# Kernel optimization log

Hardware: AMD Instinct MI355X
Metric: run time of the kernel (lower is better)

## Reference

```python
import jax, jax.numpy as jnp
import numpy as np
from jax import lax

B, T, N, F, K = 8, 16, 1024, 128, 4


def setup_inputs() -> dict:
    key = jax.random.key(0)
    k1, k2, k3, k4 = jax.random.split(key, 4)
    x = jax.random.normal(k1, (B, T, N, F), dtype=jnp.float32)
    # shift operator scaled so its spectral radius is ~1 (stable powers L^1..L^K)
    L = jax.random.normal(k2, (N, N), dtype=jnp.float32) / jnp.sqrt(jnp.float32(N))
    # xavier_uniform with relu gain: limit = gain * sqrt(6/(fan_in+fan_out))
    gain = jnp.sqrt(jnp.float32(2.0))
    lim = gain * jnp.sqrt(6.0 / (F + F))
    W = jax.random.uniform(k3, (K, F, F), dtype=jnp.float32, minval=-lim, maxval=lim)
    H = jax.random.uniform(k4, (K, F, F), dtype=jnp.float32, minval=-lim, maxval=lim)
    return {"x": x, "L": L, "W": W, "H": H}


def reference(x, L, W, H):
    """Recurrent graph-polynomial filter.

    h_t = relu( sum_{k=0}^{K-1} L^{k+1} @ (x_t @ W[k] + h_{t-1} @ H[k]) ), h_{-1}=0.
    Matches the torch loop where alpha_k starts at L and is multiplied by L each tap.
    """
    Kt = W.shape[0]
    # powers L^1 .. L^K, stacked [K, N, N]
    pows = [L]
    for _ in range(1, Kt):
        pows.append(pows[-1] @ L)
    Lp = jnp.stack(pows)

    def step(h, x_t):
        # x_t, h: [B, N, F]
        s = jnp.einsum('bnf,kfg->kbng', x_t, W) + jnp.einsum('bnf,kfg->kbng', h, H)
        z = jnp.einsum('knm,kbmg->bng', Lp, s)
        h_new = jax.nn.relu(z)
        return h_new, h_new

    xT = jnp.swapaxes(x, 0, 1)          # [T, B, N, F]
    h0 = jnp.zeros_like(x[:, 0])        # [B, N, F]
    _, outs = lax.scan(step, h0, xT)    # [T, B, N, F]
    return jnp.swapaxes(outs, 0, 1)     # [B, T, N, F]
```

## Files before the change

kernel.cpp:

```cpp
#include <hip/hip_runtime.h>
#include <stdint.h>


typedef __bf16 bf16_t;
typedef __bf16 bf16x4 __attribute__((ext_vector_type(4)));
typedef __bf16 bf16x8 __attribute__((ext_vector_type(8)));
typedef float  f32x4  __attribute__((ext_vector_type(4)));

__device__ __forceinline__ void gload_lds16(const void* g, void* l) {
    __builtin_amdgcn_global_load_lds(
        (const __attribute__((address_space(1))) void*)g,
        (__attribute__((address_space(3))) void*)l,
        16, 0, 0);
}


__global__ void k_convert_x(const float* __restrict__ xin,
                            bf16_t* __restrict__ xb, int n4) {
    int i = blockIdx.x * 256 + threadIdx.x;
    int stride = gridDim.x * 256;
    for (; i < n4; i += stride) {
        float4 v = reinterpret_cast<const float4*>(xin)[i];
        bf16x4 o = { (bf16_t)v.x, (bf16_t)v.y, (bf16_t)v.z, (bf16_t)v.w };
        reinterpret_cast<bf16x4*>(xb)[i] = o;
    }
}

__global__ void k_setup_L(const float* __restrict__ L,
                          bf16_t* __restrict__ Lcat,
                          bf16_t* __restrict__ Lt) {
    int idx = blockIdx.x * 256 + threadIdx.x;
    int n = idx >> 10, m = idx & 1023;
    float v = L[idx];
    Lcat[n * 4096 + m] = (bf16_t)v;
    Lt[m * 1024 + n]   = (bf16_t)v;
}

__global__ void k_setup_WH(const float* __restrict__ W,
                           const float* __restrict__ H,
                           bf16_t* __restrict__ WHT) {
    int idx = blockIdx.x * 256 + threadIdx.x;
    int k = idx >> 14, f = (idx >> 7) & 127, g = idx & 127;
    WHT[(k * 128 + g) * 256 + f]       = (bf16_t)W[idx];
    WHT[(k * 128 + g) * 256 + 128 + f] = (bf16_t)H[idx];
}


__global__ __launch_bounds__(256)
void k_combine(const float* __restrict__ Zp,
               bf16_t* __restrict__ h, float* __restrict__ out, int t) {
    int i = blockIdx.x * 256 + threadIdx.x;
    int n  = i >> 8;
    int cg = (i & 255) * 4;
    size_t o = (size_t)n * 1024 + cg;
    float4 v0 = *reinterpret_cast<const float4*>(Zp + o);
    float4 v1 = *reinterpret_cast<const float4*>(Zp + 1048576 + o);
    float4 v2 = *reinterpret_cast<const float4*>(Zp + 2097152 + o);
    float4 v3 = *reinterpret_cast<const float4*>(Zp + 3145728 + o);
    float4 s;
    s.x = fmaxf(v0.x + v1.x + v2.x + v3.x, 0.f);
    s.y = fmaxf(v0.y + v1.y + v2.y + v3.y, 0.f);
    s.z = fmaxf(v0.z + v1.z + v2.z + v3.z, 0.f);
    s.w = fmaxf(v0.w + v1.w + v2.w + v3.w, 0.f);
    int b = cg >> 7, g = cg & 127;
    size_t ho = (size_t)b * 131072 + (size_t)n * 128 + g;
    bf16x4 hb = { (bf16_t)s.x, (bf16_t)s.y, (bf16_t)s.z, (bf16_t)s.w };
    *reinterpret_cast<bf16x4*>(h + ho) = hb;
    *reinterpret_cast<float4*>(out + (size_t)b * 2097152
                                   + (size_t)t * 131072
                                   + (size_t)n * 128 + g) = s;
}

template<int BM, int BN, int EPI, int BADDR, int ZK>
__global__ __launch_bounds__(256)
void k_gemm(const bf16_t* __restrict__ A, int lda,
            const bf16_t* __restrict__ BT, int ldbt,
            const bf16_t* __restrict__ B2,
            int Ktot,
            bf16_t* __restrict__ Cb, float* __restrict__ Cf,
            int ldc, int t)
{
    constexpr int BK = 64;
    constexpr int WM = BM / 2, WN = BN / 2;
    constexpr int MF = WM / 16, NF = WN / 16;
    constexpr int ACH = BM * 8;
    constexpr int BCH = BN * 8;

    __shared__ __align__(16) bf16_t As[2][BM * BK];
    __shared__ __align__(16) bf16_t Bs[2][BN * BK];

    const int tid  = threadIdx.x;
    const int lane = tid & 63;
    const int wave = tid >> 6;
    const int wm = wave >> 1, wn = wave & 1;
    const int m0 = blockIdx.y * BM;
    const int c0 = blockIdx.x * BN;
    const int kb_ = blockIdx.z;

    const bf16_t* Ap = (EPI == 1) ? (A + kb_ * 128 * 256) : A;

    f32x4 acc[MF][NF] = {};

    const int NT = Ktot / BK;

    auto stage = [&](int bufi, int kt) {
        const int q0 = kt * BK + (ZK > 0 ? kb_ * ZK : 0);
        #pragma unroll
        for (int i = 0; i < ACH / 256; ++i) {
            int chunk = i * 256 + tid;
            int off = chunk * 16;
            int row = off >> 7;
            int kel = ((off ^ ((row & 7) << 4)) & 127) >> 1;
            const bf16_t* src = Ap + (size_t)(m0 + row) * lda + (q0 + kel);
            gload_lds16(src, (char*)(&As[bufi][0]) + off);
        }
        #pragma unroll
        for (int i = 0; i < BCH / 256; ++i) {
            int chunk = i * 256 + tid;
            int off = chunk * 16;
            int row = off >> 7;
            int kel = ((off ^ ((row & 7) << 4)) & 127) >> 1;
            int c = c0 + row;
            const bf16_t* src;
            if (BADDR == 0) {
                src = BT + (size_t)c * ldbt + (q0 + kel);
            } else {
                int f = q0 + kel;
                if (q0 < 128) {
                    src = BT + (size_t)(c >> 10) * 2097152
                             + (size_t)t * 131072
                             + (size_t)(c & 1023) * 128 + f;
                } else {
                    src = B2 + (size_t)c * 128 + (f - 128);
                }
            }
            gload_lds16(src, (char*)(&Bs[bufi][0]) + off);
        }
    };

    stage(0, 0);
    asm volatile("s_waitcnt vmcnt(0)" ::: "memory");
    __syncthreads();

    for (int kt = 0; kt < NT; ++kt) {
        int cur = kt & 1;
        if (kt + 1 < NT) stage(cur ^ 1, kt + 1);

        #pragma unroll
        for (int kk = 0; kk < 2; ++kk) {
            bf16x8 af[MF], bfr[NF];
            const int klane = (kk * 32 + (lane >> 4) * 8) * 2;
            #pragma unroll
            for (int mf = 0; mf < MF; ++mf) {
                int row = wm * WM + mf * 16 + (lane & 15);
                int bo = (row * 128 + klane) ^ ((row & 7) << 4);
                af[mf] = *reinterpret_cast<const bf16x8*>(
                             (const char*)(&As[cur][0]) + bo);
            }
            #pragma unroll
            for (int nf = 0; nf < NF; ++nf) {
                int row = wn * WN + nf * 16 + (lane & 15);
                int bo = (row * 128 + klane) ^ ((row & 7) << 4);
                bfr[nf] = *reinterpret_cast<const bf16x8*>(
                              (const char*)(&Bs[cur][0]) + bo);
            }
            #pragma unroll
            for (int mf = 0; mf < MF; ++mf)
                #pragma unroll
                for (int nf = 0; nf < NF; ++nf)
                    acc[mf][nf] = __builtin_amdgcn_mfma_f32_16x16x32_bf16(
                        af[mf], bfr[nf], acc[mf][nf], 0, 0, 0);
        }

        asm volatile("s_waitcnt vmcnt(0)" ::: "memory");
        __syncthreads();
    }

    #pragma unroll
    for (int mf = 0; mf < MF; ++mf) {
        #pragma unroll
        for (int nf = 0; nf < NF; ++nf) {
            f32x4 v = acc[mf][nf];
            int col   = c0 + wn * WN + nf * 16 + (lane & 15);
            int rbase = m0 + wm * WM + mf * 16 + ((lane >> 4) * 4);
            #pragma unroll
            for (int r = 0; r < 4; ++r) {
                int row = rbase + r;
                float val = v[r];
                if (EPI == 0) {
                    Cb[(size_t)row * ldc + col] = (bf16_t)val;
                } else if (EPI == 1) {
                    Cb[(size_t)(col >> 10) * 524288 + (size_t)row * 4096
                       + (size_t)kb_ * 1024 + (col & 1023)] = (bf16_t)val;
                } else if (EPI == 2) {
                    val = fmaxf(val, 0.f);
                    int b = col >> 7, g = col & 127;
                    Cb[(size_t)b * 131072 + (size_t)row * 128 + g] = (bf16_t)val;
                    Cf[(size_t)b * 2097152 + (size_t)t * 131072
                       + (size_t)row * 128 + g] = val;
                } else {
                    Cf[(size_t)kb_ * 1048576 + (size_t)row * 1024 + col] = val;
                }
            }
        }
    }
}


extern "C" void kernel_launch(void* const* d_in, const int* in_sizes, int n_in,
                              void* d_out, int out_size, void* d_ws, size_t ws_size,
                              hipStream_t stream) {
    const float* x = (const float*)d_in[0];
    const float* L = (const float*)d_in[1];
    const float* W = (const float*)d_in[2];
    const float* H = (const float*)d_in[3];
    float* out = (float*)d_out;

    char* ws = (char*)d_ws;
    bf16_t* xb   = (bf16_t*)(ws);
    bf16_t* Lcat = (bf16_t*)(ws + 33554432);
    bf16_t* Lt   = (bf16_t*)(ws + 41943040);
    bf16_t* WHT  = (bf16_t*)(ws + 44040192);
    bf16_t* Sbuf = (bf16_t*)(ws + 44302336);
    bf16_t* h    = (bf16_t*)(ws + 52690944);
    float*  Zp   = (float*) (ws + 54788096);
    if (ws_size < 54788096u) return;
    const bool bigws = (ws_size >= 71565312u);

    hipMemsetAsync(h, 0, 2097152, stream);
    k_convert_x<<<4096, 256, 0, stream>>>(x, xb, 16777216 / 4);
    k_setup_L <<<4096, 256, 0, stream>>>(L, Lcat, Lt);
    k_setup_WH<<<256, 256, 0, stream>>>(W, H, WHT);

    for (int p = 1; p < 4; ++p) {
        k_gemm<64, 64, 0, 0, 0><<<dim3(16, 16, 1), 256, 0, stream>>>(
            Lcat + (p - 1) * 1024, 4096, Lt, 1024, nullptr,
            1024, Lcat + p * 1024, nullptr, 4096, 0);
    }

    for (int t = 0; t < 16; ++t) {
        k_gemm<64, 128, 1, 1, 0><<<dim3(64, 2, 4), 256, 0, stream>>>(
            WHT, 256, xb, 0, h,
            256, Sbuf, nullptr, 0, t);
        if (bigws) {
            k_gemm<64, 128, 3, 0, 1024><<<dim3(8, 16, 4), 256, 0, stream>>>(
                Lcat, 4096, Sbuf, 4096, nullptr,
                1024, nullptr, Zp, 0, t);
            k_combine<<<1024, 256, 0, stream>>>(Zp, h, out, t);
        } else {
            k_gemm<64, 128, 2, 0, 0><<<dim3(8, 16, 1), 256, 0, stream>>>(
                Lcat, 4096, Sbuf, 4096, nullptr,
                4096, h, out, 0, t);
        }
    }
}
```

Before: 544.2 us.

## Load GEMM fragments directly from global memory with register double-buffering and XCD swizzle

```diff
diff --git a/kernel.cpp b/kernel.cpp
--- a/kernel.cpp
+++ b/kernel.cpp
@@ -6,13 +6,6 @@
 typedef __bf16 bf16x4 __attribute__((ext_vector_type(4)));
 typedef __bf16 bf16x8 __attribute__((ext_vector_type(8)));
 typedef float  f32x4  __attribute__((ext_vector_type(4)));
-
-__device__ __forceinline__ void gload_lds16(const void* g, void* l) {
-    __builtin_amdgcn_global_load_lds(
-        (const __attribute__((address_space(1))) void*)g,
-        (__attribute__((address_space(3))) void*)l,
-        16, 0, 0);
-}
 
 
 __global__ void k_convert_x(const float* __restrict__ xin,
@@ -71,109 +64,112 @@
                                    + (size_t)n * 128 + g) = s;
 }
 
-template<int BM, int BN, int EPI, int BADDR, int ZK>
+template<int BM, int BN, int GX, int GY, int GZ, int KTOT,
+         int EPI, int BADDR, int ZK, int DEC>
 __global__ __launch_bounds__(256)
 void k_gemm(const bf16_t* __restrict__ A, int lda,
             const bf16_t* __restrict__ BT, int ldbt,
             const bf16_t* __restrict__ B2,
-            int Ktot,
             bf16_t* __restrict__ Cb, float* __restrict__ Cf,
             int ldc, int t)
 {
     constexpr int BK = 64;
     constexpr int WM = BM / 2, WN = BN / 2;
     constexpr int MF = WM / 16, NF = WN / 16;
-    constexpr int ACH = BM * 8;
-    constexpr int BCH = BN * 8;
-
-    __shared__ __align__(16) bf16_t As[2][BM * BK];
-    __shared__ __align__(16) bf16_t Bs[2][BN * BK];
+    constexpr int NT = KTOT / BK;
+    constexpr int NWG = GX * GY * GZ;
 
     const int tid  = threadIdx.x;
     const int lane = tid & 63;
     const int wave = tid >> 6;
     const int wm = wave >> 1, wn = wave & 1;
-    const int m0 = blockIdx.y * BM;
-    const int c0 = blockIdx.x * BN;
-    const int kb_ = blockIdx.z;
+
+    const int id  = blockIdx.x;
+    const int swz = (id & 7) * (NWG / 8) + (id >> 3);
+    int bx, by, bz;
+    if (DEC == 0) {
+        bx = swz % GX; by = (swz / GX) % GY; bz = swz / (GX * GY);
+    } else {
+        by = swz % GY; bz = (swz / GY) % GZ; bx = swz / (GY * GZ);
+    }
+
+    const int m0 = by * BM;
+    const int c0 = bx * BN;
+    const int kb_ = bz;
 
     const bf16_t* Ap = (EPI == 1) ? (A + kb_ * 128 * 256) : A;
+    const int q0base = (ZK > 0) ? kb_ * ZK : 0;
+
+    const int lane15 = lane & 15;
+    const int ksub   = (lane >> 4) * 8;
+
+    uint32_t offA[MF];
+    #pragma unroll
+    for (int mf = 0; mf < MF; ++mf) {
+        uint32_t row = (uint32_t)(m0 + wm * WM + mf * 16 + lane15);
+        offA[mf] = row * (uint32_t)lda + (uint32_t)(q0base + ksub);
+    }
+    uint32_t offB[NF], offBx[NF], offBh[NF];
+    #pragma unroll
+    for (int nf = 0; nf < NF; ++nf) {
+        uint32_t c = (uint32_t)(c0 + wn * WN + nf * 16 + lane15);
+        if (BADDR == 0) {
+            offB[nf] = c * (uint32_t)ldbt + (uint32_t)(q0base + ksub);
+            offBx[nf] = 0; offBh[nf] = 0;
+        } else {
+            offB[nf] = 0;
+            offBx[nf] = (c >> 10) * 2097152u + (uint32_t)t * 131072u
+                      + (c & 1023u) * 128u + (uint32_t)ksub;
+            offBh[nf] = c * 128u + (uint32_t)ksub;
+        }
+    }
+
+    auto ldA = [&](int mf, int tile, int kk) -> bf16x8 {
+        return *reinterpret_cast<const bf16x8*>(
+            Ap + offA[mf] + (uint32_t)(tile * 64 + kk * 32));
+    };
+    auto ldB = [&](int nf, int tile, int kk) -> bf16x8 {
+        if constexpr (BADDR == 0) {
+            return *reinterpret_cast<const bf16x8*>(
+                BT + offB[nf] + (uint32_t)(tile * 64 + kk * 32));
+        } else {
+            if (tile < NT / 2)
+                return *reinterpret_cast<const bf16x8*>(
+                    BT + offBx[nf] + (uint32_t)(tile * 64 + kk * 32));
+            return *reinterpret_cast<const bf16x8*>(
+                B2 + offBh[nf] + (uint32_t)((tile - NT / 2) * 64 + kk * 32));
+        }
+    };
 
     f32x4 acc[MF][NF] = {};
-
-    const int NT = Ktot / BK;
-
-    auto stage = [&](int bufi, int kt) {
-        const int q0 = kt * BK + (ZK > 0 ? kb_ * ZK : 0);
-        #pragma unroll
-        for (int i = 0; i < ACH / 256; ++i) {
-            int chunk = i * 256 + tid;
-            int off = chunk * 16;
-            int row = off >> 7;
-            int kel = ((off ^ ((row & 7) << 4)) & 127) >> 1;
-            const bf16_t* src = Ap + (size_t)(m0 + row) * lda + (q0 + kel);
-            gload_lds16(src, (char*)(&As[bufi][0]) + off);
-        }
-        #pragma unroll
-        for (int i = 0; i < BCH / 256; ++i) {
-            int chunk = i * 256 + tid;
-            int off = chunk * 16;
-            int row = off >> 7;
-            int kel = ((off ^ ((row & 7) << 4)) & 127) >> 1;
-            int c = c0 + row;
-            const bf16_t* src;
-            if (BADDR == 0) {
-                src = BT + (size_t)c * ldbt + (q0 + kel);
-            } else {
-                int f = q0 + kel;
-                if (q0 < 128) {
-                    src = BT + (size_t)(c >> 10) * 2097152
-                             + (size_t)t * 131072
-                             + (size_t)(c & 1023) * 128 + f;
-                } else {
-                    src = B2 + (size_t)c * 128 + (f - 128);
-                }
-            }
-            gload_lds16(src, (char*)(&Bs[bufi][0]) + off);
-        }
-    };
-
-    stage(0, 0);
-    asm volatile("s_waitcnt vmcnt(0)" ::: "memory");
-    __syncthreads();
-
-    for (int kt = 0; kt < NT; ++kt) {
-        int cur = kt & 1;
-        if (kt + 1 < NT) stage(cur ^ 1, kt + 1);
-
+    bf16x8 a0[MF][2], b0[NF][2], a1[MF][2], b1[NF][2];
+
+    auto loadT = [&](bf16x8 (&fa)[MF][2], bf16x8 (&fb)[NF][2], int tile) {
         #pragma unroll
         for (int kk = 0; kk < 2; ++kk) {
-            bf16x8 af[MF], bfr[NF];
-            const int klane = (kk * 32 + (lane >> 4) * 8) * 2;
-            #pragma unroll
-            for (int mf = 0; mf < MF; ++mf) {
-                int row = wm * WM + mf * 16 + (lane & 15);
-                int bo = (row * 128 + klane) ^ ((row & 7) << 4);
-                af[mf] = *reinterpret_cast<const bf16x8*>(
-                             (const char*)(&As[cur][0]) + bo);
-            }
-            #pragma unroll
-            for (int nf = 0; nf < NF; ++nf) {
-                int row = wn * WN + nf * 16 + (lane & 15);
-                int bo = (row * 128 + klane) ^ ((row & 7) << 4);
-                bfr[nf] = *reinterpret_cast<const bf16x8*>(
-                              (const char*)(&Bs[cur][0]) + bo);
-            }
+            #pragma unroll
+            for (int mf = 0; mf < MF; ++mf) fa[mf][kk] = ldA(mf, tile, kk);
+            #pragma unroll
+            for (int nf = 0; nf < NF; ++nf) fb[nf][kk] = ldB(nf, tile, kk);
+        }
+    };
+    auto mfmaT = [&](bf16x8 (&fa)[MF][2], bf16x8 (&fb)[NF][2]) {
+        #pragma unroll
+        for (int kk = 0; kk < 2; ++kk)
             #pragma unroll
             for (int mf = 0; mf < MF; ++mf)
                 #pragma unroll
                 for (int nf = 0; nf < NF; ++nf)
                     acc[mf][nf] = __builtin_amdgcn_mfma_f32_16x16x32_bf16(
-                        af[mf], bfr[nf], acc[mf][nf], 0, 0, 0);
-        }
-
-        asm volatile("s_waitcnt vmcnt(0)" ::: "memory");
-        __syncthreads();
+                        fa[mf][kk], fb[nf][kk], acc[mf][nf], 0, 0, 0);
+    };
+
+    loadT(a0, b0, 0);
+    for (int kt = 0; kt < NT; kt += 2) {
+        loadT(a1, b1, kt + 1);
+        mfmaT(a0, b0);
+        if (kt + 2 < NT) loadT(a0, b0, kt + 2);
+        mfmaT(a1, b1);
     }
 
     #pragma unroll
@@ -181,7 +177,7 @@
         #pragma unroll
         for (int nf = 0; nf < NF; ++nf) {
             f32x4 v = acc[mf][nf];
-            int col   = c0 + wn * WN + nf * 16 + (lane & 15);
+            int col   = c0 + wn * WN + nf * 16 + lane15;
             int rbase = m0 + wm * WM + mf * 16 + ((lane >> 4) * 4);
             #pragma unroll
             for (int r = 0; r < 4; ++r) {
@@ -233,24 +229,24 @@
     k_setup_WH<<<256, 256, 0, stream>>>(W, H, WHT);
 
     for (int p = 1; p < 4; ++p) {
-        k_gemm<64, 64, 0, 0, 0><<<dim3(16, 16, 1), 256, 0, stream>>>(
+        k_gemm<64, 64, 16, 16, 1, 1024, 0, 0, 0, 0><<<256, 256, 0, stream>>>(
             Lcat + (p - 1) * 1024, 4096, Lt, 1024, nullptr,
-            1024, Lcat + p * 1024, nullptr, 4096, 0);
+            Lcat + p * 1024, nullptr, 4096, 0);
     }
 
     for (int t = 0; t < 16; ++t) {
-        k_gemm<64, 128, 1, 1, 0><<<dim3(64, 2, 4), 256, 0, stream>>>(
+        k_gemm<64, 128, 64, 2, 4, 256, 1, 1, 0, 1><<<512, 256, 0, stream>>>(
             WHT, 256, xb, 0, h,
-            256, Sbuf, nullptr, 0, t);
+            Sbuf, nullptr, 0, t);
         if (bigws) {
-            k_gemm<64, 128, 3, 0, 1024><<<dim3(8, 16, 4), 256, 0, stream>>>(
+            k_gemm<64, 128, 8, 16, 4, 1024, 3, 0, 1024, 0><<<512, 256, 0, stream>>>(
                 Lcat, 4096, Sbuf, 4096, nullptr,
-                1024, nullptr, Zp, 0, t);
+                nullptr, Zp, 0, t);
             k_combine<<<1024, 256, 0, stream>>>(Zp, h, out, t);
         } else {
-            k_gemm<64, 128, 2, 0, 0><<<dim3(8, 16, 1), 256, 0, stream>>>(
+            k_gemm<64, 128, 8, 16, 1, 4096, 2, 0, 0, 0><<<128, 256, 0, stream>>>(
                 Lcat, 4096, Sbuf, 4096, nullptr,
-                4096, h, out, 0, t);
-        }
-    }
-}
+                h, out, 0, t);
+        }
+    }
+}
```

Measured after the change: 1.127 ms. 107% more time.

## Switch GEMMs to 32x32 MFMA, larger tiles, 8-way split-K and XCD swizzle

Applied to the files above, without the earlier changes.

```diff
diff --git a/kernel.cpp b/kernel.cpp
--- a/kernel.cpp
+++ b/kernel.cpp
@@ -6,6 +6,7 @@
 typedef __bf16 bf16x4 __attribute__((ext_vector_type(4)));
 typedef __bf16 bf16x8 __attribute__((ext_vector_type(8)));
 typedef float  f32x4  __attribute__((ext_vector_type(4)));
+typedef float  f32x16 __attribute__((ext_vector_type(16)));
 
 __device__ __forceinline__ void gload_lds16(const void* g, void* l) {
     __builtin_amdgcn_global_load_lds(
@@ -46,6 +47,7 @@
 }
 
 
+template<int NZ>
 __global__ __launch_bounds__(256)
 void k_combine(const float* __restrict__ Zp,
                bf16_t* __restrict__ h, float* __restrict__ out, int t) {
@@ -53,15 +55,14 @@
     int n  = i >> 8;
     int cg = (i & 255) * 4;
     size_t o = (size_t)n * 1024 + cg;
-    float4 v0 = *reinterpret_cast<const float4*>(Zp + o);
-    float4 v1 = *reinterpret_cast<const float4*>(Zp + 1048576 + o);
-    float4 v2 = *reinterpret_cast<const float4*>(Zp + 2097152 + o);
-    float4 v3 = *reinterpret_cast<const float4*>(Zp + 3145728 + o);
-    float4 s;
-    s.x = fmaxf(v0.x + v1.x + v2.x + v3.x, 0.f);
-    s.y = fmaxf(v0.y + v1.y + v2.y + v3.y, 0.f);
-    s.z = fmaxf(v0.z + v1.z + v2.z + v3.z, 0.f);
-    s.w = fmaxf(v0.w + v1.w + v2.w + v3.w, 0.f);
+    float4 s = *reinterpret_cast<const float4*>(Zp + o);
+    #pragma unroll
+    for (int z = 1; z < NZ; ++z) {
+        float4 v = *reinterpret_cast<const float4*>(Zp + (size_t)z * 1048576 + o);
+        s.x += v.x; s.y += v.y; s.z += v.z; s.w += v.w;
+    }
+    s.x = fmaxf(s.x, 0.f); s.y = fmaxf(s.y, 0.f);
+    s.z = fmaxf(s.z, 0.f); s.w = fmaxf(s.w, 0.f);
     int b = cg >> 7, g = cg & 127;
     size_t ho = (size_t)b * 131072 + (size_t)n * 128 + g;
     bf16x4 hb = { (bf16_t)s.x, (bf16_t)s.y, (bf16_t)s.z, (bf16_t)s.w };
@@ -71,18 +72,20 @@
                                    + (size_t)n * 128 + g) = s;
 }
 
-template<int BM, int BN, int EPI, int BADDR, int ZK>
+template<int BM, int BN, int GX, int GY, int GZ, int KTOT,
+         int EPI, int BADDR, int ZK, int DEC>
 __global__ __launch_bounds__(256)
 void k_gemm(const bf16_t* __restrict__ A, int lda,
             const bf16_t* __restrict__ BT, int ldbt,
             const bf16_t* __restrict__ B2,
-            int Ktot,
             bf16_t* __restrict__ Cb, float* __restrict__ Cf,
             int ldc, int t)
 {
     constexpr int BK = 64;
     constexpr int WM = BM / 2, WN = BN / 2;
-    constexpr int MF = WM / 16, NF = WN / 16;
+    constexpr int MF = WM / 32, NF = WN / 32;
+    constexpr int NT = KTOT / BK;
+    constexpr int NWG = GX * GY * GZ;
     constexpr int ACH = BM * 8;
     constexpr int BCH = BN * 8;
 
@@ -93,15 +96,23 @@
     const int lane = tid & 63;
     const int wave = tid >> 6;
     const int wm = wave >> 1, wn = wave & 1;
-    const int m0 = blockIdx.y * BM;
-    const int c0 = blockIdx.x * BN;
-    const int kb_ = blockIdx.z;
+
+    const int id  = blockIdx.x;
+    const int swz = (id & 7) * (NWG / 8) + (id >> 3);
+    int bx, by, bz;
+    if (DEC == 0) {
+        bx = swz % GX; by = (swz / GX) % GY; bz = swz / (GX * GY);
+    } else {
+        by = swz % GY; bz = (swz / GY) % GZ; bx = swz / (GY * GZ);
+    }
+
+    const int m0 = by * BM;
+    const int c0 = bx * BN;
+    const int kb_ = bz;
 
     const bf16_t* Ap = (EPI == 1) ? (A + kb_ * 128 * 256) : A;
 
-    f32x4 acc[MF][NF] = {};
-
-    const int NT = Ktot / BK;
+    f32x16 acc[MF][NF] = {};
 
     auto stage = [&](int bufi, int kt) {
         const int q0 = kt * BK + (ZK > 0 ? kb_ * ZK : 0);
@@ -147,19 +158,19 @@
         if (kt + 1 < NT) stage(cur ^ 1, kt + 1);
 
         #pragma unroll
-        for (int kk = 0; kk < 2; ++kk) {
+        for (int kk = 0; kk < 4; ++kk) {
             bf16x8 af[MF], bfr[NF];
-            const int klane = (kk * 32 + (lane >> 4) * 8) * 2;
+            const int klane = kk * 32 + (lane >> 5) * 16;
             #pragma unroll
             for (int mf = 0; mf < MF; ++mf) {
-                int row = wm * WM + mf * 16 + (lane & 15);
+                int row = wm * WM + mf * 32 + (lane & 31);
                 int bo = (row * 128 + klane) ^ ((row & 7) << 4);
                 af[mf] = *reinterpret_cast<const bf16x8*>(
                              (const char*)(&As[cur][0]) + bo);
             }
             #pragma unroll
             for (int nf = 0; nf < NF; ++nf) {
-                int row = wn * WN + nf * 16 + (lane & 15);
+                int row = wn * WN + nf * 32 + (lane & 31);
                 int bo = (row * 128 + klane) ^ ((row & 7) << 4);
                 bfr[nf] = *reinterpret_cast<const bf16x8*>(
                               (const char*)(&Bs[cur][0]) + bo);
@@ -168,7 +179,7 @@
             for (int mf = 0; mf < MF; ++mf)
                 #pragma unroll
                 for (int nf = 0; nf < NF; ++nf)
-                    acc[mf][nf] = __builtin_amdgcn_mfma_f32_16x16x32_bf16(
+                    acc[mf][nf] = __builtin_amdgcn_mfma_f32_32x32x16_bf16(
                         af[mf], bfr[nf], acc[mf][nf], 0, 0, 0);
         }
 
@@ -180,12 +191,12 @@
     for (int mf = 0; mf < MF; ++mf) {
         #pragma unroll
         for (int nf = 0; nf < NF; ++nf) {
-            f32x4 v = acc[mf][nf];
-            int col   = c0 + wn * WN + nf * 16 + (lane & 15);
-            int rbase = m0 + wm * WM + mf * 16 + ((lane >> 4) * 4);
-            #pragma unroll
-            for (int r = 0; r < 4; ++r) {
-                int row = rbase + r;
+            f32x16 v = acc[mf][nf];
+            int col   = c0 + wn * WN + nf * 32 + (lane & 31);
+            int rbase = m0 + wm * WM + mf * 32 + 4 * (lane >> 5);
+            #pragma unroll
+            for (int r = 0; r < 16; ++r) {
+                int row = rbase + (r & 3) + 8 * (r >> 2);
                 float val = v[r];
                 if (EPI == 0) {
                     Cb[(size_t)row * ldc + col] = (bf16_t)val;
@@ -225,7 +236,7 @@
     bf16_t* h    = (bf16_t*)(ws + 52690944);
     float*  Zp   = (float*) (ws + 54788096);
     if (ws_size < 54788096u) return;
-    const bool bigws = (ws_size >= 71565312u);
+    const bool bigws = (ws_size >= 88342528u);
 
     hipMemsetAsync(h, 0, 2097152, stream);
     k_convert_x<<<4096, 256, 0, stream>>>(x, xb, 16777216 / 4);
@@ -233,24 +244,24 @@
     k_setup_WH<<<256, 256, 0, stream>>>(W, H, WHT);
 
     for (int p = 1; p < 4; ++p) {
-        k_gemm<64, 64, 0, 0, 0><<<dim3(16, 16, 1), 256, 0, stream>>>(
+        k_gemm<64, 64, 16, 16, 1, 1024, 0, 0, 0, 0><<<256, 256, 0, stream>>>(
             Lcat + (p - 1) * 1024, 4096, Lt, 1024, nullptr,
-            1024, Lcat + p * 1024, nullptr, 4096, 0);
+            Lcat + p * 1024, nullptr, 4096, 0);
     }
 
     for (int t = 0; t < 16; ++t) {
-        k_gemm<64, 128, 1, 1, 0><<<dim3(64, 2, 4), 256, 0, stream>>>(
+        k_gemm<64, 128, 64, 2, 4, 256, 1, 1, 0, 1><<<512, 256, 0, stream>>>(
             WHT, 256, xb, 0, h,
-            256, Sbuf, nullptr, 0, t);
+            Sbuf, nullptr, 0, t);
         if (bigws) {
-            k_gemm<64, 128, 3, 0, 1024><<<dim3(8, 16, 4), 256, 0, stream>>>(
+            k_gemm<128, 128, 8, 8, 8, 512, 3, 0, 512, 0><<<512, 256, 0, stream>>>(
                 Lcat, 4096, Sbuf, 4096, nullptr,
-                1024, nullptr, Zp, 0, t);
-            k_combine<<<1024, 256, 0, stream>>>(Zp, h, out, t);
+                nullptr, Zp, 0, t);
+            k_combine<8><<<1024, 256, 0, stream>>>(Zp, h, out, t);
         } else {
-            k_gemm<64, 128, 2, 0, 0><<<dim3(8, 16, 1), 256, 0, stream>>>(
+            k_gemm<128, 128, 8, 8, 1, 4096, 2, 0, 0, 0><<<64, 256, 0, stream>>>(
                 Lcat, 4096, Sbuf, 4096, nullptr,
-                4096, h, out, 0, t);
-        }
-    }
-}
+                h, out, 0, t);
+        }
+    }
+}
```

Measured after the change: 558.9 us. 1.03x slower.
